# Optimization experiments

Measured on AMD Instinct MI355X. Metric: run time of the kernel, lower is better.

## Reference

```python
import jax, jax.numpy as jnp
import numpy as np

EPS = 1e-4  # performer softmax-kernel stabilizer
LN_EPS = 1e-5


def _layernorm(x, g, b):
    m = jnp.mean(x, axis=-1, keepdims=True)
    v = jnp.mean(jnp.square(x - m), axis=-1, keepdims=True)
    return (x - m) * jax.lax.rsqrt(v + LN_EPS) * g + b


def _softmax_features(x, proj, is_query):
    # FAVOR+ positive softmax-kernel features. x: [B,H,N,Dh], proj: [M,Dh]
    d = x.shape[-1]
    xn = x * (d ** -0.25)                      # data normalizer d^{-1/4}
    u = jnp.einsum('bhnd,md->bhnm', xn, proj)  # [B,H,N,M]
    diag = 0.5 * jnp.sum(jnp.square(xn), axis=-1, keepdims=True)
    if is_query:
        stab = jnp.max(u, axis=-1, keepdims=True)
    else:
        stab = jnp.max(u, axis=(-2, -1), keepdims=True)
    ratio = proj.shape[0] ** -0.5
    return ratio * (jnp.exp(u - diag - stab) + EPS)


def reference(x, proj, ln1_g, ln1_b, ln2_g, ln2_b, W1, b1, W2, b2):
    B, N, E = x.shape
    M, Dh = proj.shape
    H = E // Dh

    # --- multi-head fast attention sublayer (pre-LN, q=k=v, no dropout) ---
    h = _layernorm(x, ln1_g, ln1_b)
    qkv = h.reshape(B, N, H, Dh).transpose(0, 2, 1, 3)     # [B,H,N,Dh]
    q_p = _softmax_features(qkv, proj, is_query=True)      # [B,H,N,M]
    k_p = _softmax_features(qkv, proj, is_query=False)     # [B,H,N,M]

    # non-causal linear attention: O(N*M*Dh)
    k_sum = jnp.sum(k_p, axis=-2)                          # [B,H,M]
    d_inv = 1.0 / jnp.einsum('bhnm,bhm->bhn', q_p, k_sum)  # [B,H,N]
    ctx = jnp.einsum('bhnm,bhnd->bhmd', k_p, qkv)          # [B,H,M,Dh]
    attn = jnp.einsum('bhnm,bhmd,bhn->bhnd', q_p, ctx, d_inv)
    attn = attn.transpose(0, 2, 1, 3).reshape(B, N, E)
    x = x + attn

    # --- MLP sublayer (pre-LN, GELU, dropout off in eval) ---
    h2 = _layernorm(x, ln2_g, ln2_b)
    h2 = jax.nn.gelu(h2 @ W1 + b1, approximate=False) @ W2 + b2
    return x + h2


def setup_inputs() -> dict:
    B, N, E, H, M, F = 4, 2048, 768, 12, 256, 3072
    Dh = E // H
    key = jax.random.key(0)
    ks = jax.random.split(key, 4)
    return {
        'x': jax.random.normal(ks[0], (B, N, E), jnp.float32),
        'proj': jax.random.normal(ks[1], (M, Dh), jnp.float32),
        'ln1_g': jnp.ones((E,), jnp.float32),
        'ln1_b': jnp.zeros((E,), jnp.float32),
        'ln2_g': jnp.ones((E,), jnp.float32),
        'ln2_b': jnp.zeros((E,), jnp.float32),
        'W1': jax.random.normal(ks[2], (E, F), jnp.float32) * 0.02,
        'b1': jnp.zeros((F,), jnp.float32),
        'W2': jax.random.normal(ks[3], (F, E), jnp.float32) * 0.02,
        'b2': jnp.zeros((E,), jnp.float32),
    }
```

## Files before the change

### kernel.cpp

```cpp
#include <hip/hip_runtime.h>
#include <hip/hip_bf16.h>
#include <math.h>

#define B_    4
#define N_    2048
#define E_    768
#define H_    12
#define M_    256
#define F_    3072
#define DH_   64
#define BN_   (B_ * N_)
#define BH_   (B_ * H_)
#define NSP_  16

#define EPS_F     1e-4f
#define LN_EPS_F  1e-5f
#define DNORM_F   0.35355339059327373f
#define DIAGC_F   0.0625f
#define BF16_ONES 0x3F803F80u

typedef __attribute__((ext_vector_type(8))) short bf16x8;
typedef __attribute__((ext_vector_type(4))) short s16x4;
typedef __attribute__((ext_vector_type(4))) float f32x4;

static __device__ __forceinline__ float to_f32(float v) { return v; }
static __device__ __forceinline__ float to_f32(__hip_bfloat16 v) { return __bfloat162float(v); }
static __device__ __forceinline__ short f2bf(float v) {
    __hip_bfloat16 b = __float2bfloat16(v);
    return *reinterpret_cast<short*>(&b);
}

static __device__ __forceinline__ float fast_gelu(float x) {
    float xc = fminf(fmaxf(x, -9.f), 9.f);
    float y = 0.7978845608028654f * (xc + 0.044715f * xc * xc * xc);
    float tt = __expf(-2.f * y);
    return x * __builtin_amdgcn_rcpf(1.f + tt);
}

static __device__ __forceinline__ void gld_lds16(const void* g, void* lds) {
    __builtin_amdgcn_global_load_lds((const __attribute__((address_space(1))) void*)g,
                                     (__attribute__((address_space(3))) void*)lds, 16, 0, 0);
}

struct ConvSrcs { const void* s[7]; __hip_bfloat16* d[7]; };
__global__ void small_convert_kernel(ConvSrcs cs, const unsigned* __restrict__ probe) {
    constexpr int os[8] = {0, 16384, 17152, 17920, 18688, 19456, 22528, 23296};
    int isb = (*probe == BF16_ONES);
    for (int i = blockIdx.x * blockDim.x + threadIdx.x; i < 23296;
         i += gridDim.x * blockDim.x) {
        int r = 0;
#pragma unroll
        for (int k = 1; k < 7; ++k) if (i >= os[k]) r = k;
        int j = i - os[r];
        float fv = isb ? __bfloat162float(((const __hip_bfloat16*)cs.s[r])[j])
                       : ((const float*)cs.s[r])[j];
        if (r == 0) fv *= DNORM_F;
        cs.d[r][j] = __float2bfloat16(fv);
    }
}

__global__ void convert_transpose_kernel(const void* __restrict__ src,
                                         __hip_bfloat16* __restrict__ dst,
                                         int R, int C, const unsigned* __restrict__ probe) {
    __shared__ __hip_bfloat16 tile[32][33];
    int isb = (*probe == BF16_ONES);
    int c0 = blockIdx.x * 32, r0 = blockIdx.y * 32;
    int tx = threadIdx.x & 31, ty = threadIdx.x >> 5;
    if (isb) {
        const unsigned short* s = (const unsigned short*)src;
        for (int j = 0; j < 4; ++j) {
            int r = ty + j * 8;
            ((unsigned short*)&tile[r][tx])[0] = s[(size_t)(r0 + r) * C + c0 + tx];
        }
    } else {
        const float* s = (const float*)src;
        for (int j = 0; j < 4; ++j) {
            int r = ty + j * 8;
            tile[r][tx] = __float2bfloat16(s[(size_t)(r0 + r) * C + c0 + tx]);
        }
    }
    __syncthreads();
    for (int j = 0; j < 4; ++j) {
        int r = ty + j * 8;
        dst[(size_t)(c0 + r) * R + r0 + tx] = tile[tx][r];
    }
}

__global__ void ln_kernel(const void* __restrict__ x,
                          const __hip_bfloat16* __restrict__ g,
                          const __hip_bfloat16* __restrict__ b,
                          __hip_bfloat16* __restrict__ hout,
                          float* __restrict__ diag ,
                          const unsigned* __restrict__ probe ) {
    int row = blockIdx.x;
    int t = threadIdx.x, lane = t & 63, w = t >> 6;
    __shared__ float ws4[4], wq4[4];

    int isb = probe && (*probe == BF16_ONES);
    float xv[3], s = 0.f, q = 0.f;
    if (isb) {
        const __hip_bfloat16* xr = (const __hip_bfloat16*)x + (size_t)row * E_;
#pragma unroll
        for (int i = 0; i < 3; ++i) xv[i] = __bfloat162float(xr[t + i * 256]);
    } else {
        const float* xr = (const float*)x + (size_t)row * E_;
#pragma unroll
        for (int i = 0; i < 3; ++i) xv[i] = xr[t + i * 256];
    }
#pragma unroll
    for (int i = 0; i < 3; ++i) { s += xv[i]; q += xv[i] * xv[i]; }
#pragma unroll
    for (int off = 32; off >= 1; off >>= 1) {
        s += __shfl_xor(s, off);
        q += __shfl_xor(q, off);
    }
    if (lane == 0) { ws4[w] = s; wq4[w] = q; }
    __syncthreads();
    s = ws4[0] + ws4[1] + ws4[2] + ws4[3];
    q = wq4[0] + wq4[1] + wq4[2] + wq4[3];
    float mean = s * (1.0f / E_);
    float var  = q * (1.0f / E_) - mean * mean;
    float rinv = rsqrtf(fmaxf(var, 0.0f) + LN_EPS_F);

    __hip_bfloat16* hr = hout + (size_t)row * E_;
    float hv[3];
#pragma unroll
    for (int i = 0; i < 3; ++i) {
        int e = t + i * 256;
        hv[i] = (xv[i] - mean) * rinv * __bfloat162float(g[e]) + __bfloat162float(b[e]);
        hr[e] = __float2bfloat16(hv[i]);
    }
    if (diag != nullptr) {
        float d0 = hv[0] * hv[0], d1 = hv[1] * hv[1], d2 = hv[2] * hv[2];
#pragma unroll
        for (int off = 32; off >= 1; off >>= 1) {
            d0 += __shfl_xor(d0, off);
            d1 += __shfl_xor(d1, off);
            d2 += __shfl_xor(d2, off);
        }
        if (lane == 0) {
            diag[row * H_ + w]     = DIAGC_F * d0;
            diag[row * H_ + 4 + w] = DIAGC_F * d1;
            diag[row * H_ + 8 + w] = DIAGC_F * d2;
        }
    }
}

__global__ __launch_bounds__(256) void ctx_mfma_kernel(
        const __hip_bfloat16* __restrict__ h,
        const __hip_bfloat16* __restrict__ proj,
        const float* __restrict__ diag,
        float* __restrict__ pctx, float* __restrict__ pksum,
        float* __restrict__ pmax, float* __restrict__ pvsum) {
    int sp = blockIdx.x, bh = blockIdx.y;
    int bb = bh / H_, hh = bh % H_;
    int n0 = sp * 128;
    int t = threadIdx.x, lane = t & 63, w = t >> 6;
    int lm = lane & 15, kg = lane >> 4;

    __shared__ __align__(16) short hv_s[128 * 72];
    __shared__ __align__(16) short vt_s[64 * 136];
    __shared__ __align__(16) short p_s[64 * 72];
    __shared__ __align__(16) short kpt_s[64 * 136];
    __shared__ float ksp_s[4][64];
    __shared__ float dg_s[128];
    __shared__ float wmax_s[4];
    __shared__ float vp_s[4][64];

    for (int it = 0; it < 4; ++it) {
        int c = t + it * 256; int n = c >> 3, kb = c & 7;
        uint4 vld = *(const uint4*)&h[((size_t)(bb * N_ + n0 + n)) * E_ + hh * DH_ + kb * 8];
        *(uint4*)&hv_s[n * 72 + kb * 8] = vld;
        union { uint4 u4; short sh[8]; } uu; uu.u4 = vld;
        for (int j = 0; j < 8; ++j) vt_s[(kb * 8 + j) * 136 + n] = uu.sh[j];
    }
    if (t < 128) dg_s[t] = diag[(size_t)(bb * N_ + n0 + t) * H_ + hh];
    __syncthreads();

    {
        int d = t & 63, rg = t >> 6;
        float s = 0.f;
        for (int n = rg * 32; n < rg * 32 + 32; ++n)
            s += __bfloat162float(*(const __hip_bfloat16*)&hv_s[n * 72 + d]);
        vp_s[rg][d] = s;
    }
    __syncthreads();
    if (t < 64)
        pvsum[((size_t)sp * BH_ + bh) * 64 + t] =
            vp_s[0][t] + vp_s[1][t] + vp_s[2][t] + vp_s[3][t];

    for (int q = 0; q < 4; ++q) {
        __syncthreads();
        for (int it = 0; it < 2; ++it) {
            int c = t + it * 256; int m = c >> 3, kb = c & 7;
            *(uint4*)&p_s[m * 72 + kb * 8] = *(const uint4*)&proj[(size_t)(q * 64 + m) * DH_ + kb * 8];
        }
        __syncthreads();

        f32x4 u[2][4];
        for (int i = 0; i < 2; ++i) for (int j = 0; j < 4; ++j) u[i][j] = (f32x4){0.f,0.f,0.f,0.f};
        for (int kc = 0; kc < 2; ++kc) {
            bf16x8 af[2], bf[4];
            for (int i = 0; i < 2; ++i)
                af[i] = *(const bf16x8*)&hv_s[(w * 32 + i * 16 + lm) * 72 + kc * 32 + kg * 8];
            for (int j = 0; j < 4; ++j)
                bf[j] = *(const bf16x8*)&p_s[(j * 16 + lm) * 72 + kc * 32 + kg * 8];
            for (int i = 0; i < 2; ++i)
                for (int j = 0; j < 4; ++j)
                    u[i][j] = __builtin_amdgcn_mfma_f32_16x16x32_bf16(af[i], bf[j], u[i][j], 0, 0, 0);
        }
        float lmax = -1e30f;
        for (int i = 0; i < 2; ++i) for (int j = 0; j < 4; ++j) for (int r = 0; r < 4; ++r)
            lmax = fmaxf(lmax, u[i][j][r]);
        for (int off = 32; off >= 1; off >>= 1) lmax = fmaxf(lmax, __shfl_xor(lmax, off));
        if (lane == 0) wmax_s[w] = lmax;
        __syncthreads();
        float Lmax = fmaxf(fmaxf(wmax_s[0], wmax_s[1]), fmaxf(wmax_s[2], wmax_s[3]));

        float kpart[4] = {0.f, 0.f, 0.f, 0.f};
        for (int i = 0; i < 2; ++i) {
            float dgv[4];
            for (int r = 0; r < 4; ++r) dgv[r] = dg_s[w * 32 + i * 16 + kg * 4 + r];
            for (int j = 0; j < 4; ++j) {
                s16x4 pk;
                for (int r = 0; r < 4; ++r) {
                    float val = __expf(u[i][j][r] - dgv[r] - Lmax);
                    kpart[j] += val;
                    pk[r] = f2bf(val);
                }
                *(s16x4*)&kpt_s[(j * 16 + lm) * 136 + (w * 32 + i * 16 + kg * 4)] = pk;
            }
        }
        for (int j = 0; j < 4; ++j) {
            kpart[j] += __shfl_xor(kpart[j], 16);
            kpart[j] += __shfl_xor(kpart[j], 32);
        }
        if (lane < 16)
            for (int j = 0; j < 4; ++j) ksp_s[w][j * 16 + lm] = kpart[j];
        __syncthreads();

        f32x4 c4[4];
        for (int jd = 0; jd < 4; ++jd) c4[jd] = (f32x4){0.f,0.f,0.f,0.f};
        for (int kc = 0; kc < 4; ++kc) {
            bf16x8 a = *(const bf16x8*)&kpt_s[(w * 16 + lm) * 136 + kc * 32 + kg * 8];
            for (int jd = 0; jd < 4; ++jd) {
                bf16x8 b = *(const bf16x8*)&vt_s[(jd * 16 + lm) * 136 + kc * 32 + kg * 8];
                c4[jd] = __builtin_amdgcn_mfma_f32_16x16x32_bf16(a, b, c4[jd], 0, 0, 0);
            }
        }
        size_t base = ((size_t)sp * BH_ + bh) * M_ + q * 64 + w * 16;
        for (int jd = 0; jd < 4; ++jd)
            for (int r = 0; r < 4; ++r)
                pctx[(base + kg * 4 + r) * DH_ + jd * 16 + lm] = c4[jd][r];
        if (t < 64)
            pksum[((size_t)sp * BH_ + bh) * M_ + q * 64 + t] =
                ksp_s[0][t] + ksp_s[1][t] + ksp_s[2][t] + ksp_s[3][t];
        if (t == 0) pmax[bh * 64 + sp * 4 + q] = Lmax;
    }
}

__global__ void ctx_reduce_kernel(const float* __restrict__ pctx,
                                  const float* __restrict__ pksum,
                                  const float* __restrict__ pmax,
                                  const float* __restrict__ pvsum,
                                  __hip_bfloat16* __restrict__ ctx_t,
                                  float* __restrict__ ksum) {
    int mb = blockIdx.x, bh = blockIdx.y;
    int t = threadIdx.x;
    __shared__ float hm_s;
    __shared__ float sc_s[16];
    __shared__ float vs_s[64];
    __shared__ float tr_s[64 * 65];
    if (t < 64) {
        float v = pmax[bh * 64 + t];
        for (int off = 32; off >= 1; off >>= 1) v = fmaxf(v, __shfl_xor(v, off));
        if (t == 0) hm_s = v;
        float s = 0.f;
        for (int sp = 0; sp < 16; ++sp) s += pvsum[((size_t)sp * BH_ + bh) * 64 + t];
        vs_s[t] = s;
    }
    __syncthreads();
    if (t < 16) sc_s[t] = __expf(pmax[bh * 64 + t * 4 + mb] - hm_s);
    __syncthreads();
    float scl[16];
    for (int sp = 0; sp < 16; ++sp) scl[sp] = sc_s[sp];
    int d = t & 63;
    for (int it = 0; it < 4; ++it) {
        int ml = (t >> 6) + it * 16;
        float acc = 0.f;
        for (int sp = 0; sp < 16; ++sp)
            acc += scl[sp] * pctx[(((size_t)sp * BH_ + bh) * M_ + mb * 64 + ml) * DH_ + d];
        tr_s[ml * 65 + d] = acc + EPS_F * vs_s[d];
    }
    if (t < 64) {
        float ka = 0.f;
        for (int sp = 0; sp < 16; ++sp)
            ka += scl[sp] * pksum[((size_t)sp * BH_ + bh) * M_ + mb * 64 + t];
        ksum[bh * M_ + mb * 64 + t] = ka + EPS_F * (float)N_;
    }
    __syncthreads();
    int mcol = t & 63;
    for (int jt = 0; jt < 4; ++jt) {
        int dl = (t >> 6) + jt * 16;
        ctx_t[((size_t)bh * DH_ + dl) * M_ + mb * 64 + mcol] = __float2bfloat16(tr_s[mcol * 65 + dl]);
    }
}

__global__ void sums_kernel(const __hip_bfloat16* __restrict__ ctx_t,
                            const float* __restrict__ ksum,
                            float* __restrict__ ctxsum, float* __restrict__ kssum) {
    int bh = blockIdx.x, t = threadIdx.x;
    __shared__ float red[256];
    int d = t >> 2, part = t & 3;
    float s = 0.f;
    for (int mm = part * 64; mm < part * 64 + 64; ++mm)
        s += __bfloat162float(ctx_t[((size_t)bh * DH_ + d) * M_ + mm]);
    red[t] = s;
    __syncthreads();
    if (t < 64) ctxsum[bh * 64 + t] = red[t * 4] + red[t * 4 + 1] + red[t * 4 + 2] + red[t * 4 + 3];
    __syncthreads();
    red[t] = ksum[bh * M_ + t];
    __syncthreads();
    for (int off = 128; off > 0; off >>= 1) {
        if (t < off) red[t] += red[t + off];
        __syncthreads();
    }
    if (t == 0) kssum[bh] = red[0];
}

__global__ __launch_bounds__(256) void attn_mfma_kernel(
        const __hip_bfloat16* __restrict__ h,
        const __hip_bfloat16* __restrict__ proj,
        const float* __restrict__ diag,
        const __hip_bfloat16* __restrict__ ctx_t,
        const float* __restrict__ ksum,
        const float* __restrict__ ctxsum,
        const float* __restrict__ kssum,
        const void* __restrict__ xin,
        float* __restrict__ x2,
        const unsigned* __restrict__ probe) {
    int ntile = blockIdx.x, bh = blockIdx.y;
    int bb = bh / H_, hh = bh % H_;
    int n0 = ntile * 128;
    int t = threadIdx.x, lane = t & 63, w = t >> 6;
    int lm = lane & 15, kg = lane >> 4;

    __shared__ __align__(16) short hq_s[128 * 72];
    __shared__ __align__(16) short p_s[64 * 72];
    __shared__ __align__(16) short ct_s[64 * 72];
    __shared__ __align__(16) short qp_s[128 * 72];
    __shared__ float ksum_s[256];
    __shared__ float dg_s[128];
    __shared__ float cs_s[64];
    __shared__ float kss_s;

    for (int it = 0; it < 4; ++it) {
        int c = t + it * 256; int n = c >> 3, kb = c & 7;
        *(uint4*)&hq_s[n * 72 + kb * 8] =
            *(const uint4*)&h[((size_t)(bb * N_ + n0 + n)) * E_ + hh * DH_ + kb * 8];
    }
    if (t < 128) dg_s[t] = diag[(size_t)(bb * N_ + n0 + t) * H_ + hh];
    ksum_s[t] = ksum[bh * M_ + t];
    if (t < 64) cs_s[t] = ctxsum[bh * 64 + t];
    if (t == 0) kss_s = kssum[bh];

    f32x4 o[2][4];
    float qs[2][4], mrun[2][4];
    for (int i = 0; i < 2; ++i)
        for (int jd = 0; jd < 4; ++jd) o[i][jd] = (f32x4){0.f,0.f,0.f,0.f};
    for (int i = 0; i < 2; ++i)
        for (int r = 0; r < 4; ++r) { qs[i][r] = 0.f; mrun[i][r] = -1e30f; }

    for (int mc = 0; mc < 4; ++mc) {
        __syncthreads();
        for (int it = 0; it < 2; ++it) {
            int c = t + it * 256; int m = c >> 3, kb = c & 7;
            *(uint4*)&p_s[m * 72 + kb * 8] = *(const uint4*)&proj[(size_t)(mc * 64 + m) * DH_ + kb * 8];
            *(uint4*)&ct_s[m * 72 + kb * 8] =
                *(const uint4*)&ctx_t[((size_t)bh * DH_ + m) * M_ + mc * 64 + kb * 8];
        }
        __syncthreads();

        f32x4 u[2][4];
        for (int i = 0; i < 2; ++i) for (int j = 0; j < 4; ++j) u[i][j] = (f32x4){0.f,0.f,0.f,0.f};
        for (int kc = 0; kc < 2; ++kc) {
            bf16x8 af[2], bf[4];
            for (int i = 0; i < 2; ++i)
                af[i] = *(const bf16x8*)&hq_s[(w * 32 + i * 16 + lm) * 72 + kc * 32 + kg * 8];
            for (int j = 0; j < 4; ++j)
                bf[j] = *(const bf16x8*)&p_s[(j * 16 + lm) * 72 + kc * 32 + kg * 8];
            for (int i = 0; i < 2; ++i)
                for (int j = 0; j < 4; ++j)
                    u[i][j] = __builtin_amdgcn_mfma_f32_16x16x32_bf16(af[i], bf[j], u[i][j], 0, 0, 0);
        }

        for (int i = 0; i < 2; ++i)
            for (int r = 0; r < 4; ++r) {
                float cm = fmaxf(fmaxf(u[i][0][r], u[i][1][r]), fmaxf(u[i][2][r], u[i][3][r]));
                for (int off = 8; off >= 1; off >>= 1) cm = fmaxf(cm, __shfl_xor(cm, off));
                float mnew = fmaxf(mrun[i][r], cm);
                float sc = __expf(mrun[i][r] - mnew);
                mrun[i][r] = mnew;
                qs[i][r] *= sc;
                for (int jd = 0; jd < 4; ++jd) o[i][jd][r] *= sc;
            }
        for (int i = 0; i < 2; ++i) {
            float dgv[4];
            for (int r = 0; r < 4; ++r) dgv[r] = dg_s[w * 32 + i * 16 + kg * 4 + r];
            for (int j = 0; j < 4; ++j) {
                float ksv = ksum_s[mc * 64 + j * 16 + lm];
                for (int r = 0; r < 4; ++r) {
                    float val = __expf(u[i][j][r] - dgv[r] - mrun[i][r]);
                    qs[i][r] += val * ksv;
                    qp_s[(w * 32 + i * 16 + kg * 4 + r) * 72 + j * 16 + lm] = f2bf(val);
                }
            }
        }
        __syncthreads();
        for (int kc = 0; kc < 2; ++kc) {
            bf16x8 af[2], bf[4];
            for (int i = 0; i < 2; ++i)
                af[i] = *(const bf16x8*)&qp_s[(w * 32 + i * 16 + lm) * 72 + kc * 32 + kg * 8];
            for (int jd = 0; jd < 4; ++jd)
                bf[jd] = *(const bf16x8*)&ct_s[(jd * 16 + lm) * 72 + kc * 32 + kg * 8];
            for (int i = 0; i < 2; ++i)
                for (int jd = 0; jd < 4; ++jd)
                    o[i][jd] = __builtin_amdgcn_mfma_f32_16x16x32_bf16(af[i], bf[jd], o[i][jd], 0, 0, 0);
        }
    }

    for (int i = 0; i < 2; ++i)
        for (int r = 0; r < 4; ++r)
            for (int off = 8; off >= 1; off >>= 1) qs[i][r] += __shfl_xor(qs[i][r], off);
    float kss = kss_s;
    int isb = (*probe == BF16_ONES);
    for (int i = 0; i < 2; ++i)
        for (int r = 0; r < 4; ++r) {
            float dinv = 1.0f / (qs[i][r] + EPS_F * kss);
            size_t row = (size_t)(bb * N_ + n0 + w * 32 + i * 16 + kg * 4 + r);
            for (int jd = 0; jd < 4; ++jd) {
                int dcol = jd * 16 + lm;
                float outv = (o[i][jd][r] + EPS_F * cs_s[dcol]) * dinv;
                size_t idx = row * E_ + hh * DH_ + dcol;
                float xres = isb ? __bfloat162float(((const __hip_bfloat16*)xin)[idx])
                                 : ((const float*)xin)[idx];
                x2[idx] = xres + outv;
            }
        }
}

template <int KK, int NCOLS, bool DO_GELU>
__global__ __launch_bounds__(256, 2) void mfma_mlp_kernel(
        const __hip_bfloat16* __restrict__ A,
        const __hip_bfloat16* __restrict__ Bt,
        const __hip_bfloat16* __restrict__ bias,
        const float* __restrict__ resid,
        void* __restrict__ outv,
        const unsigned* __restrict__ probe) {
    constexpr int TM = 128, TN = 128;
    constexpr int CA = TM / 16;
    constexpr int CPS = CA + TN / 16;
    constexpr int CPW = CPS / 4;
    constexpr int LBUF = CPS * 512;
    constexpr int NT = KK / 32;
    constexpr int NXB = NCOLS / TN;
    constexpr int NWG = NXB * (BN_ / TM);
    constexpr int CPX = NWG / 8;

    const int t = threadIdx.x;
    const int bid0 = blockIdx.y * NXB + blockIdx.x;
    const int bid = (bid0 & 7) * CPX + (bid0 >> 3);
    const int col0 = (bid % NXB) * TN;
    const int row0 = (bid / NXB) * TM;

    const int lane = t & 63, w = t >> 6;
    const int wr = w & 1, wc = w >> 1;
    const int lm = lane & 15, kg = lane >> 4;
    const int lp = lane ^ ((lane >> 3) & 7);
    const int lr = lp >> 2, lc = (lp & 3) * 8;
    const int sxa = (lm >> 1) << 3;

    __shared__ __align__(16) short Ls[2 * LBUF];

    const __hip_bfloat16* gp[CPW];
    int lof[CPW];
#pragma unroll
    for (int cc = 0; cc < CPW; ++cc) {
        int c = w + cc * 4;
        gp[cc] = (c < CA) ? &A[(size_t)(row0 + c * 16 + lr) * KK + lc]
                          : &Bt[(size_t)(col0 + (c - CA) * 16 + lr) * KK + lc];
        lof[cc] = c * 512;
    }

    f32x4 acc[4][4];
#pragma unroll
    for (int i = 0; i < 4; ++i)
#pragma unroll
        for (int j = 0; j < 4; ++j)
            acc[i][j] = (f32x4){0.f, 0.f, 0.f, 0.f};

    const int fro = (lm * 32 + kg * 8) ^ sxa;

#pragma unroll
    for (int cc = 0; cc < CPW; ++cc) gld_lds16(gp[cc], &Ls[lof[cc]]);

    int cur = 0;
    for (int ts = 0; ts < NT; ++ts) {
        if (ts + 1 < NT) {
            const int nb = (cur ^ 1) * LBUF;
            const int ko = (ts + 1) * 32;
#pragma unroll
            for (int cc = 0; cc < CPW; ++cc)
                gld_lds16(gp[cc] + ko, &Ls[nb + lof[cc]]);
            asm volatile("s_waitcnt vmcnt(%0)" :: "n"(CPW) : "memory");
        } else {
            asm volatile("s_waitcnt vmcnt(0)" ::: "memory");
        }
        __builtin_amdgcn_s_barrier();

        const short* base = &Ls[cur * LBUF];
        bf16x8 af[4], bfr[4];
#pragma unroll
        for (int i = 0; i < 4; ++i)
            af[i] = *(const bf16x8*)&base[(wr * 4 + i) * 512 + fro];
#pragma unroll
        for (int j = 0; j < 4; ++j)
            bfr[j] = *(const bf16x8*)&base[(CA + wc * 4 + j) * 512 + fro];

        asm volatile("s_waitcnt lgkmcnt(0)" ::: "memory");
        __builtin_amdgcn_sched_barrier(0);
        __builtin_amdgcn_s_barrier();

#pragma unroll
        for (int i = 0; i < 4; ++i)
#pragma unroll
            for (int j = 0; j < 4; ++j)
                acc[i][j] = __builtin_amdgcn_mfma_f32_16x16x32_bf16(af[i], bfr[j], acc[i][j], 0, 0, 0);
        cur ^= 1;
    }

    int ob = DO_GELU ? 1 : (*probe == BF16_ONES);
#pragma unroll
    for (int i = 0; i < 4; ++i) {
#pragma unroll
        for (int r = 0; r < 4; ++r) {
            int row = row0 + wr * 64 + i * 16 + kg * 4 + r;
            size_t rb = (size_t)row * NCOLS;
#pragma unroll
            for (int j = 0; j < 4; ++j) {
                int col = col0 + wc * 64 + j * 16 + lm;
                float v = acc[i][j][r] + __bfloat162float(bias[col]);
                if (DO_GELU) {
                    v = fast_gelu(v);
                } else {
                    v += resid[rb + col];
                }
                if (ob) ((__hip_bfloat16*)outv)[rb + col] = __float2bfloat16(v);
                else    ((float*)outv)[rb + col] = v;
            }
        }
    }
}

extern "C" void kernel_launch(void* const* d_in, const int* in_sizes, int n_in,
                              void* d_out, int out_size, void* d_ws, size_t ws_size,
                              hipStream_t stream) {
    char* ws = (char*)d_ws;
    size_t off = 0;
    auto carve = [&](size_t bytes) -> void* {
        void* p = ws + off;
        off += (bytes + 255) & ~(size_t)255;
        return p;
    };
    float*          x2    = (float*)carve((size_t)BN_ * E_ * 4);
    __hip_bfloat16* h     = (__hip_bfloat16*)carve((size_t)BN_ * E_ * 2);
    __hip_bfloat16* Wt1   = (__hip_bfloat16*)carve((size_t)E_ * F_ * 2);
    __hip_bfloat16* Wt2   = (__hip_bfloat16*)carve((size_t)F_ * E_ * 2);
    __hip_bfloat16* projc = (__hip_bfloat16*)carve((size_t)M_ * DH_ * 2);
    __hip_bfloat16* g1c   = (__hip_bfloat16*)carve((size_t)E_ * 2);
    __hip_bfloat16* b1lc  = (__hip_bfloat16*)carve((size_t)E_ * 2);
    __hip_bfloat16* g2c   = (__hip_bfloat16*)carve((size_t)E_ * 2);
    __hip_bfloat16* b2lc  = (__hip_bfloat16*)carve((size_t)E_ * 2);
    __hip_bfloat16* bb1c  = (__hip_bfloat16*)carve((size_t)F_ * 2);
    __hip_bfloat16* bb2c  = (__hip_bfloat16*)carve((size_t)E_ * 2);
    size_t mark = off;
    float*          diag  = (float*)carve((size_t)BN_ * H_ * 4);
    float*          pctx  = (float*)carve((size_t)NSP_ * BH_ * M_ * DH_ * 4);
    float*          pksum = (float*)carve((size_t)NSP_ * BH_ * M_ * 4);
    float*          pmax  = (float*)carve((size_t)BH_ * 64 * 4);
    float*          pvsum = (float*)carve((size_t)NSP_ * BH_ * 64 * 4);
    __hip_bfloat16* ctx_t = (__hip_bfloat16*)carve((size_t)BH_ * DH_ * M_ * 2);
    float*          ksum  = (float*)carve((size_t)BH_ * M_ * 4);
    float*          ctxsum= (float*)carve((size_t)BH_ * DH_ * 4);
    float*          kssum = (float*)carve((size_t)BH_ * 4);
    __hip_bfloat16* h2    = h;
    __hip_bfloat16* mid   = (__hip_bfloat16*)(ws + mark);

    const unsigned* probe = (const unsigned*)d_in[2];

    ConvSrcs cs;
    cs.s[0] = d_in[1]; cs.d[0] = projc;
    cs.s[1] = d_in[2]; cs.d[1] = g1c;
    cs.s[2] = d_in[3]; cs.d[2] = b1lc;
    cs.s[3] = d_in[4]; cs.d[3] = g2c;
    cs.s[4] = d_in[5]; cs.d[4] = b2lc;
    cs.s[5] = d_in[7]; cs.d[5] = bb1c;
    cs.s[6] = d_in[9]; cs.d[6] = bb2c;
    small_convert_kernel<<<91, 256, 0, stream>>>(cs, probe);
    convert_transpose_kernel<<<dim3(F_ / 32, E_ / 32), 256, 0, stream>>>(d_in[6], Wt1, E_, F_, probe);
    convert_transpose_kernel<<<dim3(E_ / 32, F_ / 32), 256, 0, stream>>>(d_in[8], Wt2, F_, E_, probe);

    ln_kernel<<<BN_, 256, 0, stream>>>(d_in[0], g1c, b1lc, h, diag, probe);
    ctx_mfma_kernel<<<dim3(NSP_, BH_), 256, 0, stream>>>(h, projc, diag, pctx, pksum, pmax, pvsum);
    ctx_reduce_kernel<<<dim3(4, BH_), 1024, 0, stream>>>(pctx, pksum, pmax, pvsum, ctx_t, ksum);
    sums_kernel<<<BH_, 256, 0, stream>>>(ctx_t, ksum, ctxsum, kssum);
    attn_mfma_kernel<<<dim3(16, BH_), 256, 0, stream>>>(h, projc, diag, ctx_t, ksum, ctxsum, kssum,
                                                        d_in[0], x2, probe);

    ln_kernel<<<BN_, 256, 0, stream>>>(x2, g2c, b2lc, h2, nullptr, nullptr);
    mfma_mlp_kernel<E_, F_, true><<<dim3(F_ / 128, BN_ / 128), 256, 0, stream>>>(
        h2, Wt1, bb1c, nullptr, (void*)mid, probe);
    mfma_mlp_kernel<F_, E_, false><<<dim3(E_ / 128, BN_ / 128), 256, 0, stream>>>(
        mid, Wt2, bb2c, x2, d_out, probe);
}
```

Measured before the change: 333.5 us.

## Store partial ctx in bf16 and fold sums kernel into attention kernel

Partial context accumulators written by the ctx kernel are now stored as bf16 instead of fp32, halving the traffic between the ctx and reduce kernels. The separate sums kernel is removed; the attention kernel now computes the column sums of ctx from its shared-memory tiles and reduces ksum with wave shuffles. This saves a launch and a small global round-trip. In exchange, partial sums lose precision and some redundant summation work is repeated per attention block.

```diff
diff --git a/kernel.cpp b/kernel.cpp
--- a/kernel.cpp
+++ b/kernel.cpp
@@ -28,6 +28,9 @@
 static __device__ __forceinline__ short f2bf(float v) {
     __hip_bfloat16 b = __float2bfloat16(v);
     return *reinterpret_cast<short*>(&b);
+}
+static __device__ __forceinline__ float bf2f(short v) {
+    return __bfloat162float(*reinterpret_cast<__hip_bfloat16*>(&v));
 }
 
 static __device__ __forceinline__ float fast_gelu(float x) {
@@ -150,7 +153,7 @@
         const __hip_bfloat16* __restrict__ h,
         const __hip_bfloat16* __restrict__ proj,
         const float* __restrict__ diag,
-        float* __restrict__ pctx, float* __restrict__ pksum,
+        __hip_bfloat16* __restrict__ pctx, float* __restrict__ pksum,
         float* __restrict__ pmax, float* __restrict__ pvsum) {
     int sp = blockIdx.x, bh = blockIdx.y;
     int bb = bh / H_, hh = bh % H_;
@@ -251,7 +254,7 @@
         size_t base = ((size_t)sp * BH_ + bh) * M_ + q * 64 + w * 16;
         for (int jd = 0; jd < 4; ++jd)
             for (int r = 0; r < 4; ++r)
-                pctx[(base + kg * 4 + r) * DH_ + jd * 16 + lm] = c4[jd][r];
+                pctx[(base + kg * 4 + r) * DH_ + jd * 16 + lm] = __float2bfloat16(c4[jd][r]);
         if (t < 64)
             pksum[((size_t)sp * BH_ + bh) * M_ + q * 64 + t] =
                 ksp_s[0][t] + ksp_s[1][t] + ksp_s[2][t] + ksp_s[3][t];
@@ -259,7 +262,7 @@
     }
 }
 
-__global__ void ctx_reduce_kernel(const float* __restrict__ pctx,
+__global__ void ctx_reduce_kernel(const __hip_bfloat16* __restrict__ pctx,
                                   const float* __restrict__ pksum,
                                   const float* __restrict__ pmax,
                                   const float* __restrict__ pvsum,
@@ -289,7 +292,8 @@
         int ml = (t >> 6) + it * 16;
         float acc = 0.f;
         for (int sp = 0; sp < 16; ++sp)
-            acc += scl[sp] * pctx[(((size_t)sp * BH_ + bh) * M_ + mb * 64 + ml) * DH_ + d];
+            acc += scl[sp] * __bfloat162float(
+                pctx[(((size_t)sp * BH_ + bh) * M_ + mb * 64 + ml) * DH_ + d]);
         tr_s[ml * 65 + d] = acc + EPS_F * vs_s[d];
     }
     if (t < 64) {
@@ -304,28 +308,6 @@
         int dl = (t >> 6) + jt * 16;
         ctx_t[((size_t)bh * DH_ + dl) * M_ + mb * 64 + mcol] = __float2bfloat16(tr_s[mcol * 65 + dl]);
     }
-}
-
-__global__ void sums_kernel(const __hip_bfloat16* __restrict__ ctx_t,
-                            const float* __restrict__ ksum,
-                            float* __restrict__ ctxsum, float* __restrict__ kssum) {
-    int bh = blockIdx.x, t = threadIdx.x;
-    __shared__ float red[256];
-    int d = t >> 2, part = t & 3;
-    float s = 0.f;
-    for (int mm = part * 64; mm < part * 64 + 64; ++mm)
-        s += __bfloat162float(ctx_t[((size_t)bh * DH_ + d) * M_ + mm]);
-    red[t] = s;
-    __syncthreads();
-    if (t < 64) ctxsum[bh * 64 + t] = red[t * 4] + red[t * 4 + 1] + red[t * 4 + 2] + red[t * 4 + 3];
-    __syncthreads();
-    red[t] = ksum[bh * M_ + t];
-    __syncthreads();
-    for (int off = 128; off > 0; off >>= 1) {
-        if (t < off) red[t] += red[t + off];
-        __syncthreads();
-    }
-    if (t == 0) kssum[bh] = red[0];
 }
 
 __global__ __launch_bounds__(256) void attn_mfma_kernel(
@@ -334,8 +316,6 @@
         const float* __restrict__ diag,
         const __hip_bfloat16* __restrict__ ctx_t,
         const float* __restrict__ ksum,
-        const float* __restrict__ ctxsum,
-        const float* __restrict__ kssum,
         const void* __restrict__ xin,
         float* __restrict__ x2,
         const unsigned* __restrict__ probe) {
@@ -352,7 +332,7 @@
     __shared__ float ksum_s[256];
     __shared__ float dg_s[128];
     __shared__ float cs_s[64];
-    __shared__ float kss_s;
+    __shared__ float km4[4];
 
     for (int it = 0; it < 4; ++it) {
         int c = t + it * 256; int n = c >> 3, kb = c & 7;
@@ -361,8 +341,7 @@
     }
     if (t < 128) dg_s[t] = diag[(size_t)(bb * N_ + n0 + t) * H_ + hh];
     ksum_s[t] = ksum[bh * M_ + t];
-    if (t < 64) cs_s[t] = ctxsum[bh * 64 + t];
-    if (t == 0) kss_s = kssum[bh];
+    if (t < 64) cs_s[t] = 0.f;
 
     f32x4 o[2][4];
     float qs[2][4], mrun[2][4];
@@ -380,6 +359,17 @@
                 *(const uint4*)&ctx_t[((size_t)bh * DH_ + m) * M_ + mc * 64 + kb * 8];
         }
         __syncthreads();
+
+        if (t < 64) {
+            float csp = 0.f;
+#pragma unroll
+            for (int mm = 0; mm < 8; ++mm) {
+                bf16x8 cv = *(const bf16x8*)&ct_s[t * 72 + mm * 8];
+#pragma unroll
+                for (int e = 0; e < 8; ++e) csp += bf2f(cv[e]);
+            }
+            cs_s[t] += csp;
+        }
 
         f32x4 u[2][4];
         for (int i = 0; i < 2; ++i) for (int j = 0; j < 4; ++j) u[i][j] = (f32x4){0.f,0.f,0.f,0.f};
@@ -429,10 +419,15 @@
         }
     }
 
+    float ks = ksum_s[t];
+    for (int off = 32; off >= 1; off >>= 1) ks += __shfl_xor(ks, off);
+    if (lane == 0) km4[w] = ks;
+    __syncthreads();
+    float kss = km4[0] + km4[1] + km4[2] + km4[3];
+
     for (int i = 0; i < 2; ++i)
         for (int r = 0; r < 4; ++r)
             for (int off = 8; off >= 1; off >>= 1) qs[i][r] += __shfl_xor(qs[i][r], off);
-    float kss = kss_s;
     int isb = (*probe == BF16_ONES);
     for (int i = 0; i < 2; ++i)
         for (int r = 0; r < 4; ++r) {
@@ -585,14 +580,12 @@
     __hip_bfloat16* bb2c  = (__hip_bfloat16*)carve((size_t)E_ * 2);
     size_t mark = off;
     float*          diag  = (float*)carve((size_t)BN_ * H_ * 4);
-    float*          pctx  = (float*)carve((size_t)NSP_ * BH_ * M_ * DH_ * 4);
+    __hip_bfloat16* pctx  = (__hip_bfloat16*)carve((size_t)NSP_ * BH_ * M_ * DH_ * 2);
     float*          pksum = (float*)carve((size_t)NSP_ * BH_ * M_ * 4);
     float*          pmax  = (float*)carve((size_t)BH_ * 64 * 4);
     float*          pvsum = (float*)carve((size_t)NSP_ * BH_ * 64 * 4);
     __hip_bfloat16* ctx_t = (__hip_bfloat16*)carve((size_t)BH_ * DH_ * M_ * 2);
     float*          ksum  = (float*)carve((size_t)BH_ * M_ * 4);
-    float*          ctxsum= (float*)carve((size_t)BH_ * DH_ * 4);
-    float*          kssum = (float*)carve((size_t)BH_ * 4);
     __hip_bfloat16* h2    = h;
     __hip_bfloat16* mid   = (__hip_bfloat16*)(ws + mark);
 
@@ -613,8 +606,7 @@
     ln_kernel<<<BN_, 256, 0, stream>>>(d_in[0], g1c, b1lc, h, diag, probe);
     ctx_mfma_kernel<<<dim3(NSP_, BH_), 256, 0, stream>>>(h, projc, diag, pctx, pksum, pmax, pvsum);
     ctx_reduce_kernel<<<dim3(4, BH_), 1024, 0, stream>>>(pctx, pksum, pmax, pvsum, ctx_t, ksum);
-    sums_kernel<<<BH_, 256, 0, stream>>>(ctx_t, ksum, ctxsum, kssum);
-    attn_mfma_kernel<<<dim3(16, BH_), 256, 0, stream>>>(h, projc, diag, ctx_t, ksum, ctxsum, kssum,
+    attn_mfma_kernel<<<dim3(16, BH_), 256, 0, stream>>>(h, projc, diag, ctx_t, ksum,
                                                         d_in[0], x2, probe);
 
     ln_kernel<<<BN_, 256, 0, stream>>>(x2, g2c, b2lc, h2, nullptr, nullptr);
```

Result: no change. 331.5 us (-0.6%).
